# Kernel tuning notes

Hardware: AMD Instinct MI355X
Metric: run time of the kernel (lower is better)

## Reference

```python
import jax, jax.numpy as jnp
import numpy as np

NC = 1      # constants.nc (Game-of-Life grid channels)
GRID = 32
PAD_ITERS = 31


def _iterated_wrap_idx(n, p):
    # Faithfully simulate p iterations of circular pad-1 on a growing axis.
    # NOTE: this is NOT a single wrap-pad of p; the border alternates 0/n-1.
    idx = np.arange(n)
    for _ in range(p):
        idx = np.concatenate([idx[-1:], idx, idx[:1]])
    return jnp.asarray(idx)

_IDX = _iterated_wrap_idx(GRID, PAD_ITERS)  # length 94, static


def _pad(x):
    # one gather per spatial dim replaces the 31-iteration concat loop
    return x[:, :, _IDX][:, :, :, _IDX]


def _conv(x, w, b, stride):
    y = jax.lax.conv_general_dilated(
        x, w, window_strides=(stride, stride), padding='VALID',
        dimension_numbers=('NCHW', 'OIHW', 'NCHW'))
    return y + b[None, :, None, None]


def setup_inputs() -> dict:
    key = jax.random.key(0)
    ks = jax.random.split(key, 7)
    B = 16
    s_in = 1.0 / np.sqrt(NC * 32 * 32)      # fan-in init, keeps activations sane
    s_hid = 1.0 / np.sqrt(32 * 32 * 32)
    s_out = 1.0 / np.sqrt(32)
    return {
        'x': jax.random.normal(ks[0], (B, NC, GRID, GRID), jnp.float32),
        'in_w': jax.random.normal(ks[1], (32, NC, 32, 32), jnp.float32) * s_in,
        'in_b': jnp.zeros((32,), jnp.float32),
        'convs_w': jax.random.normal(ks[2], (20, 32, 32, 32, 32), jnp.float32) * s_hid,
        'convs_b': jnp.zeros((20, 32), jnp.float32),
        'out_w': jax.random.normal(ks[3], (NC, 32, 1, 1), jnp.float32) * s_out,
        'out_b': jnp.zeros((NC,), jnp.float32),
    }


def reference(x, in_w, in_b, convs_w, convs_b, out_w, out_b):
    # in_conv: pad(31 iters) + conv k=32 s=2 (no ReLU, as in original)
    h = _conv(_pad(x), in_w, in_b, 2)           # [B,32,32,32]

    def step(h, wb):
        w, b = wb
        h = jax.nn.relu(_conv(_pad(h), w, b, 2))
        return h, None

    h, _ = jax.lax.scan(step, h, (convs_w, convs_b))  # 20 hidden layers
    return _conv(h, out_w, out_b, 1)             # 1x1 out conv, no activation
```

## Files before the change

kernel.cpp:

```cpp
#include <hip/hip_runtime.h>


typedef _Float16 f16;
typedef _Float16 f16x8 __attribute__((ext_vector_type(8)));
typedef float f32x4 __attribute__((ext_vector_type(4)));
typedef float f32x16 __attribute__((ext_vector_type(16)));

__device__ __forceinline__ int mwrap(int j) {
  int t = j - 31;
  if ((unsigned)t <= 31u) return t;
  if (t < 0) return (j & 1) ? 0 : 31;
  return (j & 1) ? 0 : 31;
}


#define GOLBODY(PB, AUSE)                                                   \
  {                                                                         \
    f16x8 F[6][2];                                                          \
    _Pragma("unroll")                                                       \
    for (int j_ = 0; j_ < 6; ++j_) {                                        \
      int4 t0_, t1_;                                                        \
      t0_.x = PB[j_][0]; t0_.y = PB[j_][1];                                 \
      t0_.z = PB[j_][2]; t0_.w = PB[j_][3];                                 \
      t1_.x = PB[j_][8]; t1_.y = PB[j_][9];                                 \
      t1_.z = PB[j_][10]; t1_.w = PB[j_][11];                               \
      F[j_][0] = __builtin_bit_cast(f16x8, t0_);                            \
      F[j_][1] = __builtin_bit_cast(f16x8, t1_);                            \
    }                                                                       \
    _Pragma("unroll")                                                       \
    for (int kyi_ = 0; kyi_ < 4; ++kyi_) {                                  \
      _Pragma("unroll")                                                     \
      for (int kxh_ = 0; kxh_ < 2; ++kxh_) {                                \
        const f16x8 a_ = AUSE[kyi_ * 2 + kxh_];                             \
        acc0 = __builtin_amdgcn_mfma_f32_32x32x16_f16(a_, F[kyi_][kxh_],    \
                                                      acc0, 0, 0, 0);       \
        acc1 = __builtin_amdgcn_mfma_f32_32x32x16_f16(a_, F[kyi_ + 2][kxh_],\
                                                      acc1, 0, 0, 0);       \
      }                                                                     \
    }                                                                       \
  }

#define GOLBAR()                                       \
  asm volatile("s_waitcnt lgkmcnt(0)" ::: "memory");   \
  __builtin_amdgcn_sched_barrier(0);                   \
  __builtin_amdgcn_s_barrier();

template <int CIN, bool RELU, bool PRE>
__global__ __launch_bounds__(512, 2) void gemm3(
    const void* __restrict__ Wv,
    const f16* __restrict__ hp_in,
    const float* __restrict__ bias,
    f16* __restrict__ hp_out) {
  __shared__ __align__(16) f16 rowbuf[4][32][96];
  __shared__ float Red[8][2][1024];

  const int tid = threadIdx.x;
  const int lane = tid & 63;
  const int w = tid >> 6;
  const int ox = lane & 31;
  const int s = lane >> 5;

  const int pair0 = blockIdx.x * 2;
  const int b = pair0 >> 5;
  const int oy0 = pair0 & 31;

  const int rrow = tid / 12, rseg = tid - rrow * 12;

  int ybase[6];
#pragma unroll
  for (int j = 0; j < 6; ++j) ybase[j] = mwrap(2 * oy0 + 4 * w + j);

  const int bi = ox + 4 * s;
  const int *P0[6], *P1[6], *P2[6], *P3[6];
#pragma unroll
  for (int j = 0; j < 6; ++j) {
    P0[j] = (const int*)(&rowbuf[0][ybase[j]][0]) + bi;
    P1[j] = (const int*)(&rowbuf[1][ybase[j]][0]) + bi;
    P2[j] = (const int*)(&rowbuf[2][ybase[j]][0]) + bi;
    P3[j] = (const int*)(&rowbuf[3][ybase[j]][0]) + bi;
  }

  f32x16 acc0 = {}, acc1 = {};
  f16x8 A0[8], A1[8];
  f16x8 stgA = {}, stgB = {};

  auto loadA = [&](int c, f16x8* dst) {
#pragma unroll
    for (int kyi = 0; kyi < 4; ++kyi) {
#pragma unroll
      for (int kxh = 0; kxh < 2; ++kxh) {
        const int ky = 4 * w + kyi;
        const int chunk = (c * 32 + ky) * 2 + kxh;
        if constexpr (PRE) {
          const f16* Wl = (const f16*)Wv;
          dst[kyi * 2 + kxh] = *(const f16x8*)(Wl + (size_t)chunk * 512 + lane * 8);
        } else {
          const float* Wl = (const float*)Wv;
          const float* sp = Wl + (((size_t)(ox * CIN + c) * 32 + ky) * 32 + kxh * 16 + s * 8);
          f32x4 u0 = *(const f32x4*)sp;
          f32x4 u1 = *(const f32x4*)(sp + 4);
          f16x8 v;
          v[0] = (f16)u0[0]; v[1] = (f16)u0[1]; v[2] = (f16)u0[2]; v[3] = (f16)u0[3];
          v[4] = (f16)u1[0]; v[5] = (f16)u1[1]; v[6] = (f16)u1[2]; v[7] = (f16)u1[3];
          dst[kyi * 2 + kxh] = v;
        }
      }
    }
  };
  auto loadRowTo = [&](int c, f16x8& dst) {
    if (tid < 384)
      dst = *(const f16x8*)(hp_in + ((size_t)(b * CIN + c) * 32 + rrow) * 96 + rseg * 8);
  };
  auto writeRow = [&](int nb, const f16x8& src) {
    if (tid < 384) *(f16x8*)(&rowbuf[nb][rrow][rseg * 8]) = src;
  };

  if constexpr (CIN == 1) {
    loadRowTo(0, stgA);
    writeRow(0, stgA);
    loadA(0, A0);
    __syncthreads();
    GOLBODY(P0, A0);
  } else {
    static_assert(CIN % 4 == 0, "CIN must be 1 or multiple of 4");
    loadRowTo(0, stgA);
    loadRowTo(1, stgB);
    writeRow(0, stgA);
    writeRow(1, stgB);
    loadA(0, A0);
    __syncthreads();

#pragma unroll 1
    for (int gg = 0; gg < CIN / 4; ++gg) {
      const int c0 = 4 * gg;
      loadRowTo(c0 + 2, stgA);
      loadRowTo(c0 + 3, stgB);
      loadA(c0 + 1, A1);
      GOLBODY(P0, A0);
      loadA(c0 + 2, A0);
      GOLBODY(P1, A1);
      writeRow(2, stgA);
      writeRow(3, stgB);
      GOLBAR();
      const bool more = (c0 + 4 < CIN);
      if (more) {
        loadRowTo(c0 + 4, stgA);
        loadRowTo(c0 + 5, stgB);
      }
      loadA(c0 + 3, A1);
      GOLBODY(P2, A0);
      if (more) loadA(c0 + 4, A0);
      GOLBODY(P3, A1);
      if (more) {
        writeRow(0, stgA);
        writeRow(1, stgB);
        GOLBAR();
      }
    }
  }

#pragma unroll
  for (int r = 0; r < 16; ++r) {
    Red[w][0][r * 64 + lane] = acc0[r];
    Red[w][1][r * 64 + lane] = acc1[r];
  }
  __syncthreads();

#pragma unroll
  for (int k4 = 0; k4 < 4; ++k4) {
    const int o = tid + 512 * k4;
    const int p = o >> 10, co = (o >> 5) & 31, oxx = o & 31;
    const int idx = ((co & 3) + 4 * (co >> 3)) * 64 + ((co >> 2) & 1) * 32 + oxx;
    float v = bias[co];
#pragma unroll
    for (int w8 = 0; w8 < 8; ++w8) v += Red[w8][p][idx];
    if (RELU) v = fmaxf(v, 0.f);
    const f16 hv = (f16)v;
    f16* base = hp_out + ((size_t)(b * 32 + co) * 32 + (oy0 + p)) * 96;
    base[oxx + 31] = hv;
    if (oxx == 0) {
#pragma unroll
      for (int j = 1; j <= 29; j += 2) base[j] = hv;
#pragma unroll
      for (int j = 63; j <= 93; j += 2) base[j] = hv;
    }
    if (oxx == 31) {
#pragma unroll
      for (int j = 0; j <= 30; j += 2) base[j] = hv;
#pragma unroll
      for (int j = 64; j <= 92; j += 2) base[j] = hv;
    }
  }
}

__global__ void pad_x_kernel(const float* __restrict__ x, f16* __restrict__ xp) {
  const int i = blockIdx.x * 256 + threadIdx.x;
  if (i >= 48128) return;
  const int bq = i / 3008, r = i - bq * 3008;
  const int y = r / 94, j = r - y * 94;
  xp[bq * 3072 + y * 96 + j] = (f16)x[(bq * 32 + y) * 32 + mwrap(j)];
}

__global__ void convert_w3(const float* __restrict__ in_w,
                           const float* __restrict__ convs_w,
                           f16* __restrict__ WfIn, f16* __restrict__ WfH) {
  const int total = 4096 + 20 * 131072;
  for (int g = blockIdx.x * blockDim.x + threadIdx.x; g < total;
       g += gridDim.x * blockDim.x) {
    const float* src;
    f16* dst;
    int chunk, lanE, c, ky, kxh;
    if (g < 4096) {
      chunk = g >> 6; lanE = g & 63;
      kxh = chunk & 1; ky = chunk >> 1; c = 0;
      const int co = lanE & 31, ss = lanE >> 5;
      src = in_w + ((size_t)(co * 1 + 0) * 32 + ky) * 32 + kxh * 16 + ss * 8;
      dst = WfIn + (size_t)chunk * 512 + lanE * 8;
    } else {
      const int h = g - 4096;
      const int layer = h >> 17, r = h & 131071;
      chunk = r >> 6; lanE = r & 63;
      kxh = chunk & 1;
      const int t = chunk >> 1;
      ky = t & 31; c = t >> 5;
      const int co = lanE & 31, ss = lanE >> 5;
      src = convs_w + (size_t)layer * 1048576 +
            ((size_t)(co * 32 + c) * 32 + ky) * 32 + kxh * 16 + ss * 8;
      dst = WfH + (size_t)layer * 1048576 + (size_t)chunk * 512 + lanE * 8;
    }
    f32x4 u0 = *(const f32x4*)src;
    f32x4 u1 = *(const f32x4*)(src + 4);
    f16x8 v;
    v[0] = (f16)u0[0]; v[1] = (f16)u0[1]; v[2] = (f16)u0[2]; v[3] = (f16)u0[3];
    v[4] = (f16)u1[0]; v[5] = (f16)u1[1]; v[6] = (f16)u1[2]; v[7] = (f16)u1[3];
    *(f16x8*)dst = v;
  }
}

__global__ void out_conv3(const f16* __restrict__ hp,
                          const float* __restrict__ ow,
                          const float* __restrict__ ob,
                          float* __restrict__ out) {
  const int o = blockIdx.x * 256 + threadIdx.x;
  const int b = o >> 10, oy = (o >> 5) & 31, oxx = o & 31;
  float s = ob[0];
#pragma unroll
  for (int c = 0; c < 32; ++c)
    s += ow[c] * (float)hp[((size_t)(b * 32 + c) * 32 + oy) * 96 + oxx + 31];
  out[o] = s;
}

extern "C" void kernel_launch(void* const* d_in, const int* in_sizes, int n_in,
                              void* d_out, int out_size, void* d_ws,
                              size_t ws_size, hipStream_t stream) {
  const float* x = (const float*)d_in[0];
  const float* in_w = (const float*)d_in[1];
  const float* in_b = (const float*)d_in[2];
  const float* convs_w = (const float*)d_in[3];
  const float* convs_b = (const float*)d_in[4];
  const float* out_w = (const float*)d_in[5];
  const float* out_b = (const float*)d_in[6];
  float* out = (float*)d_out;

  char* ws = (char*)d_ws;
  f16* xpad = (f16*)ws;
  f16* hpA = (f16*)(ws + 98304);
  f16* hpB = (f16*)(ws + 98304 + 3145728);
  f16* WfIn = (f16*)(ws + 6389760);
  f16* WfH = (f16*)(ws + 6455296);
  const bool pre = (ws_size >= 48398336ull);

  pad_x_kernel<<<188, 256, 0, stream>>>(x, xpad);
  if (pre) convert_w3<<<2048, 256, 0, stream>>>(in_w, convs_w, WfIn, WfH);

  if (pre)
    gemm3<1, false, true><<<256, 512, 0, stream>>>(WfIn, xpad, in_b, hpA);
  else
    gemm3<1, false, false><<<256, 512, 0, stream>>>(in_w, xpad, in_b, hpA);

  for (int l = 0; l < 20; ++l) {
    const f16* cur = (l % 2 == 0) ? hpA : hpB;
    f16* nxt = (l % 2 == 0) ? hpB : hpA;
    if (pre)
      gemm3<32, true, true><<<256, 512, 0, stream>>>(
          WfH + (size_t)l * 1048576, cur, convs_b + 32 * l, nxt);
    else
      gemm3<32, true, false><<<256, 512, 0, stream>>>(
          convs_w + (size_t)l * 1048576, cur, convs_b + 32 * l, nxt);
  }

  out_conv3<<<64, 256, 0, stream>>>(hpA, out_w, out_b, out);
}
```

Baseline: 948.2 us.

## Double LDS row ring to 8 slots and software-pipeline B-fragment loads

Grows the shared-memory row buffer from 4 to 8 channel slots, used as a ring, so the next four input-channel rows are staged while the current four are consumed. This allows one barrier per four channels instead of two. B fragments are now read from LDS into registers one channel ahead of the MFMA block that uses them, so LDS reads overlap matrix work. The cost is more LDS and more registers (an extra F buffer and two more staging vectors), which may lower occupancy under the 512x2 launch bounds.

After: 987.7 us. 4.2% more time.

```diff
diff --git a/kernel.cpp b/kernel.cpp
--- a/kernel.cpp
+++ b/kernel.cpp
@@ -14,27 +14,30 @@
 }
 
 
-#define GOLBODY(PB, AUSE)                                                   \
+#define LOADF(FD, cc)                                                       \
   {                                                                         \
-    f16x8 F[6][2];                                                          \
+    const int so_ = ((cc) & 7) * 6144;                                      \
     _Pragma("unroll")                                                       \
     for (int j_ = 0; j_ < 6; ++j_) {                                        \
+      const int* Rj_ = (const int*)(lds0 + V[j_] + so_);                    \
       int4 t0_, t1_;                                                        \
-      t0_.x = PB[j_][0]; t0_.y = PB[j_][1];                                 \
-      t0_.z = PB[j_][2]; t0_.w = PB[j_][3];                                 \
-      t1_.x = PB[j_][8]; t1_.y = PB[j_][9];                                 \
-      t1_.z = PB[j_][10]; t1_.w = PB[j_][11];                               \
-      F[j_][0] = __builtin_bit_cast(f16x8, t0_);                            \
-      F[j_][1] = __builtin_bit_cast(f16x8, t1_);                            \
+      t0_.x = Rj_[0]; t0_.y = Rj_[1]; t0_.z = Rj_[2]; t0_.w = Rj_[3];       \
+      t1_.x = Rj_[8]; t1_.y = Rj_[9]; t1_.z = Rj_[10]; t1_.w = Rj_[11];     \
+      FD[j_][0] = __builtin_bit_cast(f16x8, t0_);                           \
+      FD[j_][1] = __builtin_bit_cast(f16x8, t1_);                           \
     }                                                                       \
+  }
+
+#define MFMAC(AUSE, FD)                                                     \
+  {                                                                         \
     _Pragma("unroll")                                                       \
     for (int kyi_ = 0; kyi_ < 4; ++kyi_) {                                  \
       _Pragma("unroll")                                                     \
       for (int kxh_ = 0; kxh_ < 2; ++kxh_) {                                \
         const f16x8 a_ = AUSE[kyi_ * 2 + kxh_];                             \
-        acc0 = __builtin_amdgcn_mfma_f32_32x32x16_f16(a_, F[kyi_][kxh_],    \
+        acc0 = __builtin_amdgcn_mfma_f32_32x32x16_f16(a_, FD[kyi_][kxh_],   \
                                                       acc0, 0, 0, 0);       \
-        acc1 = __builtin_amdgcn_mfma_f32_32x32x16_f16(a_, F[kyi_ + 2][kxh_],\
+        acc1 = __builtin_amdgcn_mfma_f32_32x32x16_f16(a_, FD[kyi_ + 2][kxh_],\
                                                       acc1, 0, 0, 0);       \
       }                                                                     \
     }                                                                       \
@@ -51,7 +54,7 @@
     const f16* __restrict__ hp_in,
     const float* __restrict__ bias,
     f16* __restrict__ hp_out) {
-  __shared__ __align__(16) f16 rowbuf[4][32][96];
+  __shared__ __align__(16) f16 rowbuf[8][32][96];
   __shared__ float Red[8][2][1024];
 
   const int tid = threadIdx.x;
@@ -66,23 +69,19 @@
 
   const int rrow = tid / 12, rseg = tid - rrow * 12;
 
-  int ybase[6];
-#pragma unroll
-  for (int j = 0; j < 6; ++j) ybase[j] = mwrap(2 * oy0 + 4 * w + j);
-
   const int bi = ox + 4 * s;
-  const int *P0[6], *P1[6], *P2[6], *P3[6];
-#pragma unroll
-  for (int j = 0; j < 6; ++j) {
-    P0[j] = (const int*)(&rowbuf[0][ybase[j]][0]) + bi;
-    P1[j] = (const int*)(&rowbuf[1][ybase[j]][0]) + bi;
-    P2[j] = (const int*)(&rowbuf[2][ybase[j]][0]) + bi;
-    P3[j] = (const int*)(&rowbuf[3][ybase[j]][0]) + bi;
-  }
+  char* lds0 = (char*)&rowbuf[0][0][0];
+  int V[6];
+#pragma unroll
+  for (int j = 0; j < 6; ++j)
+    V[j] = mwrap(2 * oy0 + 4 * w + j) * 192 + bi * 4;
+
+  const int wroff = rrow * 192 + rseg * 16;
 
   f32x16 acc0 = {}, acc1 = {};
   f16x8 A0[8], A1[8];
-  f16x8 stgA = {}, stgB = {};
+  f16x8 F0[6][2], F1[6][2];
+  f16x8 stgA = {}, stgB = {}, stgC = {}, stgD = {};
 
   auto loadA = [&](int c, f16x8* dst) {
 #pragma unroll
@@ -111,51 +110,51 @@
     if (tid < 384)
       dst = *(const f16x8*)(hp_in + ((size_t)(b * CIN + c) * 32 + rrow) * 96 + rseg * 8);
   };
-  auto writeRow = [&](int nb, const f16x8& src) {
-    if (tid < 384) *(f16x8*)(&rowbuf[nb][rrow][rseg * 8]) = src;
+  auto writeSlot = [&](int slot, const f16x8& src) {
+    if (tid < 384) *(f16x8*)(lds0 + slot * 6144 + wroff) = src;
   };
 
   if constexpr (CIN == 1) {
     loadRowTo(0, stgA);
-    writeRow(0, stgA);
+    writeSlot(0, stgA);
     loadA(0, A0);
     __syncthreads();
-    GOLBODY(P0, A0);
+    LOADF(F0, 0);
+    MFMAC(A0, F0);
   } else {
-    static_assert(CIN % 4 == 0, "CIN must be 1 or multiple of 4");
-    loadRowTo(0, stgA);
-    loadRowTo(1, stgB);
-    writeRow(0, stgA);
-    writeRow(1, stgB);
+    static_assert(CIN % 4 == 0, "CIN must be 1 or a multiple of 4");
+    loadRowTo(0, stgA); loadRowTo(1, stgB);
+    loadRowTo(2, stgC); loadRowTo(3, stgD);
+    writeSlot(0, stgA); writeSlot(1, stgB);
+    writeSlot(2, stgC); writeSlot(3, stgD);
     loadA(0, A0);
     __syncthreads();
 
 #pragma unroll 1
-    for (int gg = 0; gg < CIN / 4; ++gg) {
-      const int c0 = 4 * gg;
-      loadRowTo(c0 + 2, stgA);
-      loadRowTo(c0 + 3, stgB);
-      loadA(c0 + 1, A1);
-      GOLBODY(P0, A0);
-      loadA(c0 + 2, A0);
-      GOLBODY(P1, A1);
-      writeRow(2, stgA);
-      writeRow(3, stgB);
+    for (int g = 0; g < CIN / 4; ++g) {
+      const int t0 = 4 * g;
+      const bool more = (t0 + 4 < CIN);
+      if (more) {
+        loadRowTo(t0 + 4, stgA); loadRowTo(t0 + 5, stgB);
+        loadRowTo(t0 + 6, stgC); loadRowTo(t0 + 7, stgD);
+      }
+      LOADF(F0, t0);
+      loadA(t0 + 1, A1);
+      LOADF(F1, t0 + 1);
+      MFMAC(A0, F0);
+      LOADF(F0, t0 + 2);
+      loadA(t0 + 2, A0);
+      MFMAC(A1, F1);
+      LOADF(F1, t0 + 3);
+      loadA(t0 + 3, A1);
+      MFMAC(A0, F0);
+      if (more) {
+        writeSlot((t0 + 4) & 7, stgA); writeSlot((t0 + 5) & 7, stgB);
+        writeSlot((t0 + 6) & 7, stgC); writeSlot((t0 + 7) & 7, stgD);
+        loadA(t0 + 4, A0);
+      }
+      MFMAC(A1, F1);
       GOLBAR();
-      const bool more = (c0 + 4 < CIN);
-      if (more) {
-        loadRowTo(c0 + 4, stgA);
-        loadRowTo(c0 + 5, stgB);
-      }
-      loadA(c0 + 3, A1);
-      GOLBODY(P2, A0);
-      if (more) loadA(c0 + 4, A0);
-      GOLBODY(P3, A1);
-      if (more) {
-        writeRow(0, stgA);
-        writeRow(1, stgB);
-        GOLBAR();
-      }
     }
   }
 
```
